# Optimization experiments

Measured on AMD Instinct MI355X. Metric: run time of the kernel, lower is better.

Reference implementation:

```python
import jax, jax.numpy as jnp
import numpy as np

B, S, D_MODEL = 1, 2048, 2048
N_HEADS, N_KV_HEADS, D_HEAD = 16, 4, 128
ROTARY_DIM, ROTARY_BASE = 128, 10000.0
ATTN_SCALE = float(np.sqrt(D_HEAD))
REPEAT = N_HEADS // N_KV_HEADS


def _sin_cos_rotary(n_ctx, rotary_dim, base):
    # TransformerLens calculate_sin_cos_rotary, rotary_adjacent_pairs=False:
    # freq repeated as 'd -> (2 d)'
    pos = jnp.arange(n_ctx, dtype=jnp.float32)
    dim = jnp.arange(rotary_dim // 2, dtype=jnp.float32)
    freq = base ** (dim / (rotary_dim / 2))
    freq = jnp.concatenate([freq, freq])  # (2 d)
    angles = pos[:, None] / freq[None, :]  # [n_ctx, rotary_dim]
    return jnp.sin(angles), jnp.cos(angles)


def _rotate_every_two_half(x):
    # rotate_half for non-adjacent pairs: [-x2, x1]
    d = x.shape[-1]
    return jnp.concatenate([-x[..., d // 2:], x[..., : d // 2]], axis=-1)


def _apply_rotary(x, sin, cos):
    # x: [batch, pos, head, d_head]; sin/cos: [n_ctx, rotary_dim]
    p = x.shape[1]
    s = sin[:p][:, None, :]  # [pos, 1, rotary_dim]
    c = cos[:p][:, None, :]
    x_rot = x[..., :ROTARY_DIM]
    x_pass = x[..., ROTARY_DIM:]
    x_rotated = x_rot * c + _rotate_every_two_half(x_rot) * s
    return jnp.concatenate([x_rotated, x_pass], axis=-1)


def setup_inputs() -> dict:
    key = jax.random.key(0)
    ks = jax.random.split(key, 10)
    init = 1.0 / np.sqrt(D_MODEL)
    return {
        "query_input": jax.random.normal(ks[0], (B, S, D_MODEL), jnp.float32),
        "key_input": jax.random.normal(ks[1], (B, S, D_MODEL), jnp.float32),
        "value_input": jax.random.normal(ks[2], (B, S, D_MODEL), jnp.float32),
        "W_Q": jax.random.normal(ks[3], (N_HEADS, D_MODEL, D_HEAD), jnp.float32) * init,
        "b_Q": jnp.zeros((N_HEADS, D_HEAD), jnp.float32),
        "W_K": jax.random.normal(ks[4], (N_KV_HEADS, D_MODEL, D_HEAD), jnp.float32) * init,
        "b_K": jnp.zeros((N_KV_HEADS, D_HEAD), jnp.float32),
        "W_V": jax.random.normal(ks[5], (N_KV_HEADS, D_MODEL, D_HEAD), jnp.float32) * init,
        "b_V": jnp.zeros((N_KV_HEADS, D_HEAD), jnp.float32),
        "W_O": jax.random.normal(ks[6], (N_HEADS, D_HEAD, D_MODEL), jnp.float32) * init,
        "b_O": jnp.zeros((D_MODEL,), jnp.float32),
    }


def reference(query_input, key_input, value_input, W_Q, b_Q, W_K, b_K, W_V, b_V, W_O, b_O):
    sin, cos = _sin_cos_rotary(S, ROTARY_DIM, ROTARY_BASE)

    # Projections
    q = jnp.einsum("bpd,hdk->bphk", query_input, W_Q) + b_Q   # [B,S,H,dh]
    k = jnp.einsum("bpd,hdk->bphk", key_input, W_K) + b_K     # [B,S,Hkv,dh]
    v = jnp.einsum("bpd,hdk->bphk", value_input, W_V) + b_V   # [B,S,Hkv,dh]

    # Rotary on q and k (before KV head expansion)
    q = _apply_rotary(q, sin, cos)
    k = _apply_rotary(k, sin, cos)

    # GQA expansion via repeat_interleave on head dim
    k = jnp.repeat(k, REPEAT, axis=2)  # [B,S,H,dh]
    v = jnp.repeat(v, REPEAT, axis=2)

    # Attention scores, causal mask, softmax
    scores = jnp.einsum("bqhd,bkhd->bhqk", q, k) / ATTN_SCALE  # [B,H,S,S]
    causal = jnp.tril(jnp.ones((S, S), dtype=bool))
    scores = jnp.where(causal, scores, jnp.finfo(scores.dtype).min)
    pattern = jax.nn.softmax(scores, axis=-1)

    # Weighted values and output projection
    z = jnp.einsum("bhqk,bkhd->bqhd", pattern, v)              # [B,S,H,dh]
    out = jnp.einsum("bqhd,hdm->bqm", z, W_O) + b_O            # [B,S,D]
    return out
```

## Files before the change

kernel.cpp:

```cpp
#include <hip/hip_runtime.h>
#include <hip/hip_bf16.h>
#include <stdint.h>
#include <math.h>

typedef __bf16 bf16_t;
typedef __attribute__((ext_vector_type(8))) __bf16 bf16x8;
typedef __attribute__((ext_vector_type(4))) __bf16 bf16x4;
typedef __attribute__((ext_vector_type(4))) float f32x4;

static constexpr int S = 2048;
static constexpr int DM = 2048;
static constexpr int NH = 16;
static constexpr int NKV = 4;
static constexpr int DH = 128;

#define MFMA16(a, b, c) __builtin_amdgcn_mfma_f32_16x16x32_bf16((a), (b), (c), 0, 0, 0)

__device__ __forceinline__ void gload_lds16(const void* g, void* l) {
  __builtin_amdgcn_global_load_lds((__attribute__((address_space(1))) void*)(g),
                                   (__attribute__((address_space(3))) void*)(l), 16, 0, 0);
}

template <int N>
__device__ __forceinline__ void wait_vmcnt() {
  asm volatile("s_waitcnt vmcnt(%0)" :: "n"(N) : "memory");
}
__device__ __forceinline__ void wait_lgkm0() {
  asm volatile("s_waitcnt lgkmcnt(0)" ::: "memory");
}

__global__ void rope_table_k(float2* __restrict__ tab) {
  int p = blockIdx.x;
  int j = threadIdx.x;
  double inv = exp2(-(double)j * 13.287712379549449 / 64.0);
  double ang = (double)p * inv;
  tab[p * 64 + j] = make_float2((float)sin(ang), (float)cos(ang));
}

__global__ void cvt3_k(const float* __restrict__ Xq, const float* __restrict__ Xk,
                       const float* __restrict__ Xv, bf16_t* __restrict__ xq,
                       bf16_t* __restrict__ xk, bf16_t* __restrict__ xv) {
  int i = (blockIdx.x * 256 + threadIdx.x) * 4;
  const float* in; bf16_t* out; int off;
  if (i < 4194304) { in = Xq; out = xq; off = i; }
  else if (i < 8388608) { in = Xk; out = xk; off = i - 4194304; }
  else { in = Xv; out = xv; off = i - 8388608; }
  f32x4 v = *(const f32x4*)(in + off);
  bf16x4 o;
  o[0] = (bf16_t)v[0]; o[1] = (bf16_t)v[1]; o[2] = (bf16_t)v[2]; o[3] = (bf16_t)v[3];
  *(bf16x4*)(out + off) = o;
}

__global__ void transpose_w_k(const float* __restrict__ in, bf16_t* __restrict__ out,
                              int R, int C, int rb, int cb, int ldo) {
  __shared__ float tile[32][33];
  int b = blockIdx.z;
  int c0 = blockIdx.x * 32, r0 = blockIdx.y * 32;
  int tx = threadIdx.x, ty = threadIdx.y;
  const float* src = in + (size_t)b * R * C;
  #pragma unroll
  for (int j = 0; j < 32; j += 8)
    tile[ty + j][tx] = src[(size_t)(r0 + ty + j) * C + c0 + tx];
  __syncthreads();
  #pragma unroll
  for (int j = 0; j < 32; j += 8) {
    int c = c0 + ty + j;
    int r = r0 + tx;
    out[(size_t)(b * rb + c) * ldo + b * cb + r] = (bf16_t)tile[tx][ty + j];
  }
}

__global__ void transpose_wkv_k(const float* __restrict__ WK, const float* __restrict__ WV,
                                bf16_t* __restrict__ wkT, bf16_t* __restrict__ wvT) {
  __shared__ float tile[32][33];
  int z = blockIdx.z;
  int b = z & 3;
  const float* in = (z < 4) ? WK : WV;
  bf16_t* out = (z < 4) ? wkT : wvT;
  int c0 = blockIdx.x * 32, r0 = blockIdx.y * 32;
  int tx = threadIdx.x, ty = threadIdx.y;
  const float* src = in + (size_t)b * 2048 * 128;
  #pragma unroll
  for (int j = 0; j < 32; j += 8)
    tile[ty + j][tx] = src[(size_t)(r0 + ty + j) * 128 + c0 + tx];
  __syncthreads();
  #pragma unroll
  for (int j = 0; j < 32; j += 8) {
    int c = c0 + ty + j;
    int r = r0 + tx;
    out[(size_t)(b * 128 + c) * 2048 + r] = (bf16_t)tile[tx][ty + j];
  }
}

__global__ void rope_qk_k(bf16_t* __restrict__ Qb, bf16_t* __restrict__ Kb,
                          const float2* __restrict__ tab, float qscale) {
  int tid = blockIdx.x * 256 + threadIdx.x;
  int row = tid >> 4;
  int i = (tid & 15) * 4;
  bf16_t* base; float scale;
  if (row < NH * S) { base = Qb + (size_t)row * DH; scale = qscale; }
  else { base = Kb + (size_t)(row - NH * S) * DH; scale = 1.0f; }
  int p = row & (S - 1);
  bf16x4 lo = *(bf16x4*)(base + i);
  bf16x4 hi = *(bf16x4*)(base + i + 64);
  float4 t0 = *(const float4*)(tab + p * 64 + i);
  float4 t1 = *(const float4*)(tab + p * 64 + i + 2);
  float sv[4] = {t0.x, t0.z, t1.x, t1.z};
  float cv[4] = {t0.y, t0.w, t1.y, t1.w};
  bf16x4 nlo, nhi;
  #pragma unroll
  for (int j = 0; j < 4; ++j) {
    float a = (float)lo[j], b = (float)hi[j];
    nlo[j] = (bf16_t)((a * cv[j] - b * sv[j]) * scale);
    nhi[j] = (bf16_t)((b * cv[j] + a * sv[j]) * scale);
  }
  *(bf16x4*)(base + i) = nlo;
  *(bf16x4*)(base + i + 64) = nhi;
}

__global__ __launch_bounds__(256)
void proj_gemm_k(const bf16_t* __restrict__ xq, const bf16_t* __restrict__ xk,
                 const bf16_t* __restrict__ xv, const bf16_t* __restrict__ wqT,
                 const bf16_t* __restrict__ wkT, const bf16_t* __restrict__ wvT,
                 const float* __restrict__ bQ, const float* __restrict__ bK,
                 const float* __restrict__ bV, bf16_t* __restrict__ Qb,
                 bf16_t* __restrict__ Kb, bf16_t* __restrict__ Vt) {
  const int nb = blockIdx.x;
  const int m0 = blockIdx.y * 128;
  const bf16_t* A; const bf16_t* B; const float* bias; bf16_t* dst; int ncol0;
  bool vmode = false;
  if (nb < 32)      { A = xq; B = wqT; bias = bQ; dst = Qb; ncol0 = nb * 64; }
  else if (nb < 40) { A = xk; B = wkT; bias = bK; dst = Kb; ncol0 = (nb - 32) * 64; }
  else              { A = xv; B = wvT; bias = bV; dst = Vt; ncol0 = (nb - 40) * 64; vmode = true; }
  const int K = 2048;
  const int t = threadIdx.x;
  const int lane = t & 63, w = t >> 6;
  const int l15 = lane & 15, lg = lane >> 4;
  const int wr = (w >> 1) * 64, wc = (w & 1) * 32;

  __shared__ bf16_t lA[2][128 * 64];
  __shared__ bf16_t lB[2][64 * 64];

  f32x4 acc[4][2] = {};
  const int srow = t >> 3;
  const int sslot = t & 7;

  auto stage = [&](int buf, int kt) {
    #pragma unroll
    for (int i = 0; i < 4; ++i) {
      int row = i * 32 + srow;
      int ss = sslot ^ (row & 7);
      gload_lds16(A + (size_t)(m0 + row) * K + kt * 64 + ss * 8,
                  (void*)(&lA[buf][0] + i * 2048 + t * 8));
    }
    #pragma unroll
    for (int i = 0; i < 2; ++i) {
      int row = i * 32 + srow;
      int ss = sslot ^ (row & 7);
      gload_lds16(B + (size_t)(ncol0 + row) * K + kt * 64 + ss * 8,
                  (void*)(&lB[buf][0] + i * 2048 + t * 8));
    }
  };

  const int nk = K >> 6;
  stage(0, 0);
  for (int kt = 0; kt < nk; ++kt) {
    const int cur = kt & 1;
    if (kt + 1 < nk) {
      stage(cur ^ 1, kt + 1);
      wait_vmcnt<6>();
    } else {
      wait_vmcnt<0>();
    }
    __builtin_amdgcn_s_barrier();
    #pragma unroll
    for (int kk = 0; kk < 2; ++kk) {
      bf16x8 af[4], bfv[2];
      #pragma unroll
      for (int f = 0; f < 4; ++f) {
        int row = wr + f * 16 + l15;
        int slot = kk * 4 + lg;
        af[f] = *(const bf16x8*)(&lA[cur][0] + row * 64 + ((slot ^ (row & 7)) * 8));
      }
      #pragma unroll
      for (int f = 0; f < 2; ++f) {
        int row = wc + f * 16 + l15;
        int slot = kk * 4 + lg;
        bfv[f] = *(const bf16x8*)(&lB[cur][0] + row * 64 + ((slot ^ (row & 7)) * 8));
      }
      #pragma unroll
      for (int fm = 0; fm < 4; ++fm)
        #pragma unroll
        for (int fn = 0; fn < 2; ++fn)
          acc[fm][fn] = MFMA16(af[fm], bfv[fn], acc[fm][fn]);
    }
    wait_lgkm0();
    __builtin_amdgcn_s_barrier();
  }

  #pragma unroll
  for (int fm = 0; fm < 4; ++fm) {
    int rowb = m0 + wr + fm * 16 + lg * 4;
    #pragma unroll
    for (int fn = 0; fn < 2; ++fn) {
      int col = ncol0 + wc + fn * 16 + l15;
      float bb = bias[col];
      if (vmode) {
        bf16x4 pk;
        #pragma unroll
        for (int r = 0; r < 4; ++r) pk[r] = (bf16_t)(acc[fm][fn][r] + bb);
        *(bf16x4*)(dst + (size_t)col * S + rowb) = pk;
      } else {
        #pragma unroll
        for (int r = 0; r < 4; ++r) {
          float v = acc[fm][fn][r] + bb;
          dst[((size_t)(col >> 7) * S + (rowb + r)) * DH + (col & 127)] = (bf16_t)v;
        }
      }
    }
  }
}

__global__ __launch_bounds__(256)
void gemm_o_k(const bf16_t* __restrict__ A, const bf16_t* __restrict__ B,
              const float* __restrict__ bias, float* __restrict__ Cout) {
  const int ncol0 = blockIdx.x * 64;
  const int m0 = blockIdx.y * 128;
  const int K = 2048;
  const int t = threadIdx.x;
  const int lane = t & 63, w = t >> 6;
  const int l15 = lane & 15, lg = lane >> 4;
  const int wr = (w >> 1) * 64, wc = (w & 1) * 32;

  __shared__ bf16_t lA[2][128 * 64];
  __shared__ bf16_t lB[2][64 * 64];

  f32x4 acc[4][2] = {};
  const int srow = t >> 3;
  const int sslot = t & 7;

  auto stage = [&](int buf, int kt) {
    #pragma unroll
    for (int i = 0; i < 4; ++i) {
      int row = i * 32 + srow;
      int ss = sslot ^ (row & 7);
      gload_lds16(A + (size_t)(m0 + row) * K + kt * 64 + ss * 8,
                  (void*)(&lA[buf][0] + i * 2048 + t * 8));
    }
    #pragma unroll
    for (int i = 0; i < 2; ++i) {
      int row = i * 32 + srow;
      int ss = sslot ^ (row & 7);
      gload_lds16(B + (size_t)(ncol0 + row) * K + kt * 64 + ss * 8,
                  (void*)(&lB[buf][0] + i * 2048 + t * 8));
    }
  };

  const int nk = K >> 6;
  stage(0, 0);
  for (int kt = 0; kt < nk; ++kt) {
    const int cur = kt & 1;
    if (kt + 1 < nk) {
      stage(cur ^ 1, kt + 1);
      wait_vmcnt<6>();
    } else {
      wait_vmcnt<0>();
    }
    __builtin_amdgcn_s_barrier();
    #pragma unroll
    for (int kk = 0; kk < 2; ++kk) {
      bf16x8 af[4], bfv[2];
      #pragma unroll
      for (int f = 0; f < 4; ++f) {
        int row = wr + f * 16 + l15;
        int slot = kk * 4 + lg;
        af[f] = *(const bf16x8*)(&lA[cur][0] + row * 64 + ((slot ^ (row & 7)) * 8));
      }
      #pragma unroll
      for (int f = 0; f < 2; ++f) {
        int row = wc + f * 16 + l15;
        int slot = kk * 4 + lg;
        bfv[f] = *(const bf16x8*)(&lB[cur][0] + row * 64 + ((slot ^ (row & 7)) * 8));
      }
      #pragma unroll
      for (int fm = 0; fm < 4; ++fm)
        #pragma unroll
        for (int fn = 0; fn < 2; ++fn)
          acc[fm][fn] = MFMA16(af[fm], bfv[fn], acc[fm][fn]);
    }
    wait_lgkm0();
    __builtin_amdgcn_s_barrier();
  }

  #pragma unroll
  for (int fm = 0; fm < 4; ++fm) {
    int rowb = m0 + wr + fm * 16 + lg * 4;
    #pragma unroll
    for (int fn = 0; fn < 2; ++fn) {
      int col = ncol0 + wc + fn * 16 + l15;
      float bb = bias[col];
      #pragma unroll
      for (int r = 0; r < 4; ++r)
        Cout[(size_t)(rowb + r) * DM + col] = acc[fm][fn][r] + bb;
    }
  }
}

__global__ __launch_bounds__(256)
void attn_k(const bf16_t* __restrict__ Q, const bf16_t* __restrict__ K,
            const bf16_t* __restrict__ Vt, bf16_t* __restrict__ Z,
            float* __restrict__ Opart, float* __restrict__ mpart,
            float* __restrict__ lpart) {
  const int bid = blockIdx.x;
  const int h = bid & 15;
  const int g = bid >> 4;
  int qb, ch;
  if (g <= 16) { qb = 31 - g; ch = 0; }
  else if (g == 17) { qb = 31; ch = 1; }
  else {
    int idx = (g - 18) >> 1;
    if (g & 1) { ch = 1; qb = 30 - idx; }
    else { ch = 0; qb = 14 - idx; }
  }
  const int q0 = qb * 64;
  const int hkv = h >> 2;
  const int t = threadIdx.x;
  const int lane = t & 63, w = t >> 6;
  const int l15 = lane & 15, lg = lane >> 4;

  __shared__ bf16_t lK[2][64 * 128];
  __shared__ bf16_t lV[2][128 * 64];
  __shared__ bf16_t lP[4][16 * 64];

  const int qrow = q0 + w * 16 + l15;
  bf16x8 qf[4];
  #pragma unroll
  for (int kk = 0; kk < 4; ++kk)
    qf[kk] = *(const bf16x8*)(Q + ((size_t)h * S + qrow) * DH + kk * 32 + lg * 8);

  auto stageKV = [&](int buf, int kt) {
    #pragma unroll
    for (int i = 0; i < 4; ++i) {
      int row = i * 16 + (t >> 4);
      int ss = (t & 15) ^ (row & 15);
      gload_lds16(K + ((size_t)hkv * S + kt * 64 + row) * DH + ss * 8,
                  (void*)(&lK[buf][0] + i * 2048 + t * 8));
    }
    #pragma unroll
    for (int i = 0; i < 4; ++i) {
      int row = i * 32 + (t >> 3);
      int ss = (t & 7) ^ (row & 7);
      gload_lds16(Vt + ((size_t)hkv * DH + row) * S + kt * 64 + ss * 8,
                  (void*)(&lV[buf][0] + i * 2048 + t * 8));
    }
  };

  f32x4 oacc[8] = {};
  float m_run = -1e30f, l_run = 0.f;

  const int kt0 = ch * 16;
  const int ktend = ch ? qb : ((qb < 15) ? qb : 15);
  stageKV(0, kt0);
  for (int kt = kt0; kt <= ktend; ++kt) {
    const int cur = (kt - kt0) & 1;
    if (kt < ktend) {
      stageKV(cur ^ 1, kt + 1);
      wait_vmcnt<8>();
    } else {
      wait_vmcnt<0>();
    }
    __builtin_amdgcn_s_barrier();

    f32x4 sacc[4] = {};
    __builtin_amdgcn_s_setprio(1);
    #pragma unroll
    for (int kk = 0; kk < 4; ++kk) {
      #pragma unroll
      for (int fm = 0; fm < 4; ++fm) {
        int row = fm * 16 + l15;
        int slot = kk * 4 + lg;
        bf16x8 kf = *(const bf16x8*)(&lK[cur][0] + row * 128 + ((slot ^ (row & 15)) * 8));
        sacc[fm] = MFMA16(kf, qf[kk], sacc[fm]);
      }
    }
    __builtin_amdgcn_s_setprio(0);

    const bool diag = (kt == qb);
    float smax = -1e30f;
    #pragma unroll
    for (int fm = 0; fm < 4; ++fm) {
      #pragma unroll
      for (int r = 0; r < 4; ++r) {
        float s = sacc[fm][r];
        if (diag) {
          int keyg = kt * 64 + fm * 16 + lg * 4 + r;
          if (keyg > qrow) s = -1e30f;
        }
        sacc[fm][r] = s;
        smax = fmaxf(smax, s);
      }
    }
    smax = fmaxf(smax, __shfl_xor(smax, 16));
    smax = fmaxf(smax, __shfl_xor(smax, 32));

    float m_new, alpha;
    bool noresc = __all(smax - m_run <= 8.0f);
    if (noresc) {
      m_new = m_run;
      alpha = 1.0f;
    } else {
      m_new = fmaxf(m_run, smax);
      alpha = exp2f(m_run - m_new);
    }

    float psum = 0.f;
    #pragma unroll
    for (int fm = 0; fm < 4; ++fm) {
      bf16x4 pk;
      #pragma unroll
      for (int r = 0; r < 4; ++r) {
        float p = exp2f(sacc[fm][r] - m_new);
        psum += p;
        pk[r] = (bf16_t)p;
      }
      int slot = fm * 2 + (lg >> 1);
      char* dst = (char*)(&lP[w][0]) + l15 * 128 + ((slot ^ (l15 & 7)) * 16) + ((lg & 1) * 8);
      *(bf16x4*)dst = pk;
    }
    psum += __shfl_xor(psum, 16);
    psum += __shfl_xor(psum, 32);
    l_run = l_run * alpha + psum;
    m_run = m_new;

    if (!noresc) {
      #pragma unroll
      for (int r = 0; r < 4; ++r) {
        float ar = __shfl(alpha, lg * 4 + r);
        #pragma unroll
        for (int n = 0; n < 8; ++n) oacc[n][r] *= ar;
      }
    }

    __builtin_amdgcn_s_setprio(1);
    #pragma unroll
    for (int kk2 = 0; kk2 < 2; ++kk2) {
      int pslot = kk2 * 4 + lg;
      bf16x8 pf = *(const bf16x8*)((char*)(&lP[w][0]) + l15 * 128 + ((pslot ^ (l15 & 7)) * 16));
      #pragma unroll
      for (int n = 0; n < 8; ++n) {
        int vrow = n * 16 + l15;
        int vslot = kk2 * 4 + lg;
        bf16x8 vf = *(const bf16x8*)(&lV[cur][0] + vrow * 64 + ((vslot ^ (vrow & 7)) * 8));
        oacc[n] = MFMA16(pf, vf, oacc[n]);
      }
    }
    __builtin_amdgcn_s_setprio(0);
    wait_lgkm0();
    __builtin_amdgcn_s_barrier();
  }

  if (qb < 16) {
    #pragma unroll
    for (int r = 0; r < 4; ++r) {
      float lr = __shfl(l_run, lg * 4 + r);
      float inv = 1.0f / lr;
      int qg = q0 + w * 16 + lg * 4 + r;
      #pragma unroll
      for (int n = 0; n < 8; ++n) {
        int d = n * 16 + l15;
        Z[(size_t)qg * DM + h * DH + d] = (bf16_t)(oacc[n][r] * inv);
      }
    }
  } else {
    const int slot = (h * 16 + (qb - 16)) * 2 + ch;
    float* Op = Opart + (size_t)slot * 8192;
    #pragma unroll
    for (int r = 0; r < 4; ++r) {
      int lr = w * 16 + lg * 4 + r;
      #pragma unroll
      for (int n = 0; n < 8; ++n)
        Op[lr * 128 + n * 16 + l15] = oacc[n][r];
    }
    if (lg == 0) {
      mpart[slot * 64 + w * 16 + l15] = m_run;
      lpart[slot * 64 + w * 16 + l15] = l_run;
    }
  }
}

__global__ void combine_k(const float* __restrict__ Opart, const float* __restrict__ mpart,
                          const float* __restrict__ lpart, bf16_t* __restrict__ Z) {
  int idx = blockIdx.x * 256 + threadIdx.x;
  int d = idx & 127;
  int r = (idx >> 7) & 63;
  int qb16 = (idx >> 13) & 15;
  int h = idx >> 17;
  int s0 = (h * 16 + qb16) * 2;
  float m0 = mpart[s0 * 64 + r], m1 = mpart[(s0 + 1) * 64 + r];
  float l0 = lpart[s0 * 64 + r], l1 = lpart[(s0 + 1) * 64 + r];
  float M = fmaxf(m0, m1);
  float a0 = exp2f(m0 - M), a1 = exp2f(m1 - M);
  float L = a0 * l0 + a1 * l1;
  float o0 = Opart[(size_t)s0 * 8192 + r * 128 + d];
  float o1 = Opart[(size_t)(s0 + 1) * 8192 + r * 128 + d];
  int qrow = (16 + qb16) * 64 + r;
  Z[(size_t)qrow * DM + h * DH + d] = (bf16_t)((a0 * o0 + a1 * o1) / L);
}

extern "C" void kernel_launch(void* const* d_in, const int* in_sizes, int n_in,
                              void* d_out, int out_size, void* d_ws, size_t ws_size,
                              hipStream_t stream) {
  (void)in_sizes; (void)n_in; (void)out_size; (void)ws_size;
  const float* Xq = (const float*)d_in[0];
  const float* Xk = (const float*)d_in[1];
  const float* Xv = (const float*)d_in[2];
  const float* WQ = (const float*)d_in[3];
  const float* bQ = (const float*)d_in[4];
  const float* WK = (const float*)d_in[5];
  const float* bK = (const float*)d_in[6];
  const float* WV = (const float*)d_in[7];
  const float* bV = (const float*)d_in[8];
  const float* WO = (const float*)d_in[9];
  const float* bO = (const float*)d_in[10];

  char* w = (char*)d_ws;
  float2* tab = (float2*)w;
  bf16_t* xq  = (bf16_t*)(w + (1 << 20));
  bf16_t* xk  = xq + 4194304;
  bf16_t* xv  = xk + 4194304;
  bf16_t* wqT = xv + 4194304;
  bf16_t* wkT = wqT + 4194304;
  bf16_t* wvT = wkT + 1048576;
  bf16_t* woT = wvT + 1048576;
  bf16_t* Qb  = woT + 4194304;
  bf16_t* Kb  = Qb + 4194304;
  bf16_t* Vtb = Kb + 1048576;
  bf16_t* Zb  = Vtb + 1048576;
  float* Opart = (float*)xq;
  float* mpart = Opart + 512 * 8192;
  float* lpart = mpart + 512 * 64;

  rope_table_k<<<dim3(S), dim3(64), 0, stream>>>(tab);
  cvt3_k<<<dim3(12288), dim3(256), 0, stream>>>(Xq, Xk, Xv, xq, xk, xv);
  transpose_w_k<<<dim3(4, 64, 16), dim3(32, 8), 0, stream>>>(WQ, wqT, 2048, 128, 128, 0, 2048);
  transpose_wkv_k<<<dim3(4, 64, 8), dim3(32, 8), 0, stream>>>(WK, WV, wkT, wvT);
  transpose_w_k<<<dim3(64, 4, 16), dim3(32, 8), 0, stream>>>(WO, woT, 128, 2048, 0, 128, 2048);

  proj_gemm_k<<<dim3(48, 16), dim3(256), 0, stream>>>(xq, xk, xv, wqT, wkT, wvT,
                                                      bQ, bK, bV, Qb, Kb, Vtb);

  const float qscale = 1.4426950408889634f / sqrtf(128.0f);
  rope_qk_k<<<dim3(2560), dim3(256), 0, stream>>>(Qb, Kb, tab, qscale);

  attn_k<<<dim3(768), dim3(256), 0, stream>>>(Qb, Kb, Vtb, Zb, Opart, mpart, lpart);
  combine_k<<<dim3(8192), dim3(256), 0, stream>>>(Opart, mpart, lpart, Zb);

  gemm_o_k<<<dim3(32, 16), dim3(256), 0, stream>>>(Zb, woT, bO, (float*)d_out);
}
```

Measured before the change: 159.3 us.

## Switch attention to 32x32 MFMA with 128-row query tiles and register-resident P

Rewrites the attention kernel to use 32x32x16 bf16 MFMA instructions, with each wave owning 32 query rows, so a block covers 128 query rows. The softmax probabilities are packed into MFMA A-fragments in registers using cvt_pk_bf16 and permlane32_swap, which removes the LDS round trip for P, and reductions use permlane swaps instead of shuffles. The work map is rebalanced through a lookup table: query blocks 8 and above are split into two KV halves, giving 384 blocks, and the combine kernel is adjusted to match. This cuts LDS traffic and instruction count but raises register pressure, which the launch bounds of two blocks per unit try to contain.

```diff
diff --git a/kernel.cpp b/kernel.cpp
--- a/kernel.cpp
+++ b/kernel.cpp
@@ -7,6 +7,8 @@
 typedef __attribute__((ext_vector_type(8))) __bf16 bf16x8;
 typedef __attribute__((ext_vector_type(4))) __bf16 bf16x4;
 typedef __attribute__((ext_vector_type(4))) float f32x4;
+typedef __attribute__((ext_vector_type(16))) float f32x16;
+typedef unsigned int uint2v __attribute__((ext_vector_type(2)));
 
 static constexpr int S = 2048;
 static constexpr int DM = 2048;
@@ -15,6 +17,7 @@
 static constexpr int DH = 128;
 
 #define MFMA16(a, b, c) __builtin_amdgcn_mfma_f32_16x16x32_bf16((a), (b), (c), 0, 0, 0)
+#define MFMA32(a, b, c) __builtin_amdgcn_mfma_f32_32x32x16_bf16((a), (b), (c), 0, 0, 0)
 
 __device__ __forceinline__ void gload_lds16(const void* g, void* l) {
   __builtin_amdgcn_global_load_lds((__attribute__((address_space(1))) void*)(g),
@@ -28,6 +31,38 @@
 __device__ __forceinline__ void wait_lgkm0() {
   asm volatile("s_waitcnt lgkmcnt(0)" ::: "memory");
 }
+
+__device__ __forceinline__ unsigned cvtpk(float lo, float hi) {
+  unsigned r;
+  asm("v_cvt_pk_bf16_f32 %0, %1, %2" : "=v"(r) : "v"(lo), "v"(hi));
+  return r;
+}
+__device__ __forceinline__ void plswap2(unsigned& a, unsigned& b) {
+  uint2v r = __builtin_amdgcn_permlane32_swap(a, b, false, false);
+  a = r[0]; b = r[1];
+}
+__device__ __forceinline__ float swapred_max(float x) {
+  uint2v r = __builtin_amdgcn_permlane32_swap(__float_as_uint(x), __float_as_uint(x), false, false);
+  return fmaxf(__uint_as_float(r[0]), __uint_as_float(r[1]));
+}
+__device__ __forceinline__ float swapred_sum(float x) {
+  uint2v r = __builtin_amdgcn_permlane32_swap(__float_as_uint(x), __float_as_uint(x), false, false);
+  return __uint_as_float(r[0]) + __uint_as_float(r[1]);
+}
+__device__ __forceinline__ bf16x8 packfrag(float a0, float a1, float a2, float a3,
+                                           float a4, float a5, float a6, float a7) {
+  unsigned w0 = cvtpk(a0, a1), w1 = cvtpk(a2, a3);
+  unsigned w2 = cvtpk(a4, a5), w3 = cvtpk(a6, a7);
+  plswap2(w0, w2); plswap2(w1, w3);
+  union { unsigned u[4]; bf16x8 v; } u;
+  u.u[0] = w0; u.u[1] = w1; u.u[2] = w2; u.u[3] = w3;
+  return u.v;
+}
+
+__device__ const unsigned char attn_map[24] = {
+  (15<<1)|0,(15<<1)|1,(7<<1)|0,(14<<1)|0,(14<<1)|1,(13<<1)|0,(13<<1)|1,(6<<1)|0,
+  (12<<1)|0,(12<<1)|1,(5<<1)|0,(11<<1)|0,(11<<1)|1,(10<<1)|0,(10<<1)|1,(9<<1)|0,
+  (9<<1)|1,(4<<1)|0,(8<<1)|0,(8<<1)|1,(3<<1)|0,(2<<1)|0,(1<<1)|0,(0<<1)|0};
 
 __global__ void rope_table_k(float2* __restrict__ tab) {
   int p = blockIdx.x;
@@ -306,7 +341,7 @@
   }
 }
 
-__global__ __launch_bounds__(256)
+__global__ __launch_bounds__(256, 2)
 void attn_k(const bf16_t* __restrict__ Q, const bf16_t* __restrict__ K,
             const bf16_t* __restrict__ Vt, bf16_t* __restrict__ Z,
             float* __restrict__ Opart, float* __restrict__ mpart,
@@ -314,29 +349,25 @@
   const int bid = blockIdx.x;
   const int h = bid & 15;
   const int g = bid >> 4;
-  int qb, ch;
-  if (g <= 16) { qb = 31 - g; ch = 0; }
-  else if (g == 17) { qb = 31; ch = 1; }
-  else {
-    int idx = (g - 18) >> 1;
-    if (g & 1) { ch = 1; qb = 30 - idx; }
-    else { ch = 0; qb = 14 - idx; }
-  }
-  const int q0 = qb * 64;
+  const int code = attn_map[g];
+  const int qb = code >> 1, ci = code & 1;
+  const bool split = qb >= 8;
+  const int kt0 = (split && ci) ? (qb + 1) : 0;
+  const int ktend = split ? (ci ? 2 * qb + 1 : qb) : 2 * qb + 1;
+  const int q0 = qb * 128;
   const int hkv = h >> 2;
   const int t = threadIdx.x;
   const int lane = t & 63, w = t >> 6;
-  const int l15 = lane & 15, lg = lane >> 4;
+  const int l31 = lane & 31, hi = lane >> 5;
+  const int qrow = q0 + w * 32 + l31;
 
   __shared__ bf16_t lK[2][64 * 128];
   __shared__ bf16_t lV[2][128 * 64];
-  __shared__ bf16_t lP[4][16 * 64];
-
-  const int qrow = q0 + w * 16 + l15;
-  bf16x8 qf[4];
-  #pragma unroll
-  for (int kk = 0; kk < 4; ++kk)
-    qf[kk] = *(const bf16x8*)(Q + ((size_t)h * S + qrow) * DH + kk * 32 + lg * 8);
+
+  bf16x8 qf[8];
+  #pragma unroll
+  for (int j = 0; j < 8; ++j)
+    qf[j] = *(const bf16x8*)(Q + ((size_t)h * S + qrow) * DH + j * 16 + hi * 8);
 
   auto stageKV = [&](int buf, int kt) {
     #pragma unroll
@@ -355,11 +386,9 @@
     }
   };
 
-  f32x4 oacc[8] = {};
-  float m_run = -1e30f, l_run = 0.f;
-
-  const int kt0 = ch * 16;
-  const int ktend = ch ? qb : ((qb < 15) ? qb : 15);
+  f32x16 oacc0 = {}, oacc1 = {}, oacc2 = {}, oacc3 = {};
+  float m_run = -3.0e3f, l_run = 0.f;
+
   stageKV(0, kt0);
   for (int kt = kt0; kt <= ktend; ++kt) {
     const int cur = (kt - kt0) & 1;
@@ -371,140 +400,146 @@
     }
     __builtin_amdgcn_s_barrier();
 
-    f32x4 sacc[4] = {};
+    f32x16 s0 = {}, s1 = {};
     __builtin_amdgcn_s_setprio(1);
     #pragma unroll
-    for (int kk = 0; kk < 4; ++kk) {
-      #pragma unroll
-      for (int fm = 0; fm < 4; ++fm) {
-        int row = fm * 16 + l15;
-        int slot = kk * 4 + lg;
-        bf16x8 kf = *(const bf16x8*)(&lK[cur][0] + row * 128 + ((slot ^ (row & 15)) * 8));
-        sacc[fm] = MFMA16(kf, qf[kk], sacc[fm]);
-      }
+    for (int j = 0; j < 8; ++j) {
+      int sIdx = j * 2 + hi;
+      int r0 = l31;
+      bf16x8 k0 = *(const bf16x8*)(&lK[cur][0] + r0 * 128 + ((sIdx ^ (r0 & 15)) * 8));
+      s0 = MFMA32(k0, qf[j], s0);
+      int r1 = 32 + l31;
+      bf16x8 k1 = *(const bf16x8*)(&lK[cur][0] + r1 * 128 + ((sIdx ^ (r1 & 15)) * 8));
+      s1 = MFMA32(k1, qf[j], s1);
     }
     __builtin_amdgcn_s_setprio(0);
 
-    const bool diag = (kt == qb);
-    float smax = -1e30f;
-    #pragma unroll
-    for (int fm = 0; fm < 4; ++fm) {
-      #pragma unroll
-      for (int r = 0; r < 4; ++r) {
-        float s = sacc[fm][r];
-        if (diag) {
-          int keyg = kt * 64 + fm * 16 + lg * 4 + r;
-          if (keyg > qrow) s = -1e30f;
-        }
-        sacc[fm][r] = s;
-        smax = fmaxf(smax, s);
-      }
-    }
-    smax = fmaxf(smax, __shfl_xor(smax, 16));
-    smax = fmaxf(smax, __shfl_xor(smax, 32));
+    if (kt >= 2 * qb) {
+      #pragma unroll
+      for (int r = 0; r < 16; ++r) {
+        int krow = kt * 64 + (r & 3) + 8 * (r >> 2) + 4 * hi;
+        if (krow > qrow) s0[r] = -1e30f;
+        if (krow + 32 > qrow) s1[r] = -1e30f;
+      }
+    }
+
+    float mxa = s0[0], mxb = s0[1], mxc = s0[2], mxd = s0[3];
+    #pragma unroll
+    for (int r = 4; r < 16; r += 4) {
+      mxa = fmaxf(mxa, s0[r]); mxb = fmaxf(mxb, s0[r + 1]);
+      mxc = fmaxf(mxc, s0[r + 2]); mxd = fmaxf(mxd, s0[r + 3]);
+    }
+    #pragma unroll
+    for (int r = 0; r < 16; r += 4) {
+      mxa = fmaxf(mxa, s1[r]); mxb = fmaxf(mxb, s1[r + 1]);
+      mxc = fmaxf(mxc, s1[r + 2]); mxd = fmaxf(mxd, s1[r + 3]);
+    }
+    float mfull = swapred_max(fmaxf(fmaxf(mxa, mxb), fmaxf(mxc, mxd)));
 
     float m_new, alpha;
-    bool noresc = __all(smax - m_run <= 8.0f);
-    if (noresc) {
-      m_new = m_run;
-      alpha = 1.0f;
-    } else {
-      m_new = fmaxf(m_run, smax);
-      alpha = exp2f(m_run - m_new);
-    }
-
-    float psum = 0.f;
-    #pragma unroll
-    for (int fm = 0; fm < 4; ++fm) {
-      bf16x4 pk;
-      #pragma unroll
-      for (int r = 0; r < 4; ++r) {
-        float p = exp2f(sacc[fm][r] - m_new);
-        psum += p;
-        pk[r] = (bf16_t)p;
-      }
-      int slot = fm * 2 + (lg >> 1);
-      char* dst = (char*)(&lP[w][0]) + l15 * 128 + ((slot ^ (l15 & 7)) * 16) + ((lg & 1) * 8);
-      *(bf16x4*)dst = pk;
-    }
-    psum += __shfl_xor(psum, 16);
-    psum += __shfl_xor(psum, 32);
-    l_run = l_run * alpha + psum;
+    bool nore = __all(mfull - m_run <= 8.0f);
+    if (nore) { m_new = m_run; alpha = 1.0f; }
+    else { m_new = fmaxf(m_run, mfull); alpha = exp2f(m_run - m_new); }
+
+    float psa = 0.f, psb = 0.f, psc = 0.f, psd = 0.f;
+    #pragma unroll
+    for (int r = 0; r < 16; r += 4) {
+      s0[r] = exp2f(s0[r] - m_new); psa += s0[r];
+      s0[r + 1] = exp2f(s0[r + 1] - m_new); psb += s0[r + 1];
+      s0[r + 2] = exp2f(s0[r + 2] - m_new); psc += s0[r + 2];
+      s0[r + 3] = exp2f(s0[r + 3] - m_new); psd += s0[r + 3];
+    }
+    #pragma unroll
+    for (int r = 0; r < 16; r += 4) {
+      s1[r] = exp2f(s1[r] - m_new); psa += s1[r];
+      s1[r + 1] = exp2f(s1[r + 1] - m_new); psb += s1[r + 1];
+      s1[r + 2] = exp2f(s1[r + 2] - m_new); psc += s1[r + 2];
+      s1[r + 3] = exp2f(s1[r + 3] - m_new); psd += s1[r + 3];
+    }
+    float lt = swapred_sum((psa + psb) + (psc + psd));
+    l_run = l_run * alpha + lt;
     m_run = m_new;
 
-    if (!noresc) {
-      #pragma unroll
-      for (int r = 0; r < 4; ++r) {
-        float ar = __shfl(alpha, lg * 4 + r);
-        #pragma unroll
-        for (int n = 0; n < 8; ++n) oacc[n][r] *= ar;
-      }
-    }
+    if (!nore) {
+      #pragma unroll
+      for (int r = 0; r < 16; ++r) {
+        int qs = (r & 3) + 8 * (r >> 2) + 4 * hi;
+        float ar = __shfl(alpha, qs);
+        oacc0[r] *= ar; oacc1[r] *= ar; oacc2[r] *= ar; oacc3[r] *= ar;
+      }
+    }
+
+    bf16x8 pa[4];
+    pa[0] = packfrag(s0[0], s0[1], s0[2], s0[3], s0[4], s0[5], s0[6], s0[7]);
+    pa[1] = packfrag(s0[8], s0[9], s0[10], s0[11], s0[12], s0[13], s0[14], s0[15]);
+    pa[2] = packfrag(s1[0], s1[1], s1[2], s1[3], s1[4], s1[5], s1[6], s1[7]);
+    pa[3] = packfrag(s1[8], s1[9], s1[10], s1[11], s1[12], s1[13], s1[14], s1[15]);
 
     __builtin_amdgcn_s_setprio(1);
-    #pragma unroll
-    for (int kk2 = 0; kk2 < 2; ++kk2) {
-      int pslot = kk2 * 4 + lg;
-      bf16x8 pf = *(const bf16x8*)((char*)(&lP[w][0]) + l15 * 128 + ((pslot ^ (l15 & 7)) * 16));
-      #pragma unroll
-      for (int n = 0; n < 8; ++n) {
-        int vrow = n * 16 + l15;
-        int vslot = kk2 * 4 + lg;
-        bf16x8 vf = *(const bf16x8*)(&lV[cur][0] + vrow * 64 + ((vslot ^ (vrow & 7)) * 8));
-        oacc[n] = MFMA16(pf, vf, oacc[n]);
-      }
-    }
+#define PVBLK(OA, db) { \
+    int dr = (db) * 32 + l31; \
+    _Pragma("unroll") \
+    for (int ks = 0; ks < 4; ++ks) { \
+      int sIdx = ks * 2 + hi; \
+      bf16x8 vf = *(const bf16x8*)(&lV[cur][0] + dr * 64 + ((sIdx ^ (dr & 7)) * 8)); \
+      OA = MFMA32(pa[ks], vf, OA); \
+    } }
+    PVBLK(oacc0, 0)
+    PVBLK(oacc1, 1)
+    PVBLK(oacc2, 2)
+    PVBLK(oacc3, 3)
+#undef PVBLK
     __builtin_amdgcn_s_setprio(0);
     wait_lgkm0();
     __builtin_amdgcn_s_barrier();
   }
 
-  if (qb < 16) {
-    #pragma unroll
-    for (int r = 0; r < 4; ++r) {
-      float lr = __shfl(l_run, lg * 4 + r);
-      float inv = 1.0f / lr;
-      int qg = q0 + w * 16 + lg * 4 + r;
-      #pragma unroll
-      for (int n = 0; n < 8; ++n) {
-        int d = n * 16 + l15;
-        Z[(size_t)qg * DM + h * DH + d] = (bf16_t)(oacc[n][r] * inv);
-      }
+  if (!split) {
+    float linv = 1.0f / l_run;
+    #pragma unroll
+    for (int r = 0; r < 16; ++r) {
+      int qs = (r & 3) + 8 * (r >> 2) + 4 * hi;
+      float lv = __shfl(linv, qs);
+      int qg = q0 + w * 32 + qs;
+      bf16_t* zp = Z + (size_t)qg * DM + h * DH + l31;
+      zp[0]  = (bf16_t)(oacc0[r] * lv);
+      zp[32] = (bf16_t)(oacc1[r] * lv);
+      zp[64] = (bf16_t)(oacc2[r] * lv);
+      zp[96] = (bf16_t)(oacc3[r] * lv);
     }
   } else {
-    const int slot = (h * 16 + (qb - 16)) * 2 + ch;
-    float* Op = Opart + (size_t)slot * 8192;
-    #pragma unroll
-    for (int r = 0; r < 4; ++r) {
-      int lr = w * 16 + lg * 4 + r;
-      #pragma unroll
-      for (int n = 0; n < 8; ++n)
-        Op[lr * 128 + n * 16 + l15] = oacc[n][r];
-    }
-    if (lg == 0) {
-      mpart[slot * 64 + w * 16 + l15] = m_run;
-      lpart[slot * 64 + w * 16 + l15] = l_run;
+    const int slot = (h * 8 + (qb - 8)) * 2 + ci;
+    float* Op = Opart + (size_t)slot * 16384;
+    #pragma unroll
+    for (int r = 0; r < 16; ++r) {
+      int qs = (r & 3) + 8 * (r >> 2) + 4 * hi;
+      float* op = Op + (w * 32 + qs) * 128 + l31;
+      op[0] = oacc0[r]; op[32] = oacc1[r]; op[64] = oacc2[r]; op[96] = oacc3[r];
+    }
+    if (lane < 32) {
+      mpart[slot * 128 + w * 32 + l31] = m_run;
+      lpart[slot * 128 + w * 32 + l31] = l_run;
     }
   }
 }
 
 __global__ void combine_k(const float* __restrict__ Opart, const float* __restrict__ mpart,
                           const float* __restrict__ lpart, bf16_t* __restrict__ Z) {
-  int idx = blockIdx.x * 256 + threadIdx.x;
-  int d = idx & 127;
-  int r = (idx >> 7) & 63;
-  int qb16 = (idx >> 13) & 15;
-  int h = idx >> 17;
-  int s0 = (h * 16 + qb16) * 2;
-  float m0 = mpart[s0 * 64 + r], m1 = mpart[(s0 + 1) * 64 + r];
-  float l0 = lpart[s0 * 64 + r], l1 = lpart[(s0 + 1) * 64 + r];
+  int tid = blockIdx.x * 256 + threadIdx.x;
+  int d = tid & 127;
+  int q = (tid >> 7) & 127;
+  int qb8 = (tid >> 14) & 7;
+  int h = tid >> 17;
+  int s0 = (h * 8 + qb8) * 2;
+  float m0 = mpart[s0 * 128 + q], m1 = mpart[(s0 + 1) * 128 + q];
+  float l0 = lpart[s0 * 128 + q], l1 = lpart[(s0 + 1) * 128 + q];
   float M = fmaxf(m0, m1);
   float a0 = exp2f(m0 - M), a1 = exp2f(m1 - M);
   float L = a0 * l0 + a1 * l1;
-  float o0 = Opart[(size_t)s0 * 8192 + r * 128 + d];
-  float o1 = Opart[(size_t)(s0 + 1) * 8192 + r * 128 + d];
-  int qrow = (16 + qb16) * 64 + r;
-  Z[(size_t)qrow * DM + h * DH + d] = (bf16_t)((a0 * o0 + a1 * o1) / L);
+  float o0 = Opart[(size_t)s0 * 16384 + q * 128 + d];
+  float o1 = Opart[(size_t)(s0 + 1) * 16384 + q * 128 + d];
+  int qg = (8 + qb8) * 128 + q;
+  Z[(size_t)qg * DM + h * DH + d] = (bf16_t)((a0 * o0 + a1 * o1) / L);
 }
 
 extern "C" void kernel_launch(void* const* d_in, const int* in_sizes, int n_in,
@@ -537,8 +572,8 @@
   bf16_t* Vtb = Kb + 1048576;
   bf16_t* Zb  = Vtb + 1048576;
   float* Opart = (float*)xq;
-  float* mpart = Opart + 512 * 8192;
-  float* lpart = mpart + 512 * 64;
+  float* mpart = (float*)xv;
+  float* lpart = mpart + 256 * 128;
 
   rope_table_k<<<dim3(S), dim3(64), 0, stream>>>(tab);
   cvt3_k<<<dim3(12288), dim3(256), 0, stream>>>(Xq, Xk, Xv, xq, xk, xv);
@@ -552,7 +587,7 @@
   const float qscale = 1.4426950408889634f / sqrtf(128.0f);
   rope_qk_k<<<dim3(2560), dim3(256), 0, stream>>>(Qb, Kb, tab, qscale);
 
-  attn_k<<<dim3(768), dim3(256), 0, stream>>>(Qb, Kb, Vtb, Zb, Opart, mpart, lpart);
+  attn_k<<<dim3(384), dim3(256), 0, stream>>>(Qb, Kb, Vtb, Zb, Opart, mpart, lpart);
   combine_k<<<dim3(8192), dim3(256), 0, stream>>>(Opart, mpart, lpart, Zb);
 
   gemm_o_k<<<dim3(32, 16), dim3(256), 0, stream>>>(Zb, woT, bO, (float*)d_out);
```

New measurement: 157.5 us. Within noise of the previous version (-1.1%).
